# Kernel optimization log

Measured on AMD Instinct MI355X. Metric: run time of the kernel, lower is better.

## Reference

```python
import jax, jax.numpy as jnp
import numpy as np

N_SRC = 100000
N_DST = 100000
N_EDGES = 640000
D = 128
D_OUT = 128


def setup_inputs() -> dict:
    key = jax.random.key(0)
    k1, k2, k3, k4, k5, k6 = jax.random.split(key, 6)
    h_src = jax.random.normal(k1, (N_SRC, D), dtype=jnp.float32)
    h_dst = jax.random.normal(k2, (N_DST, D), dtype=jnp.float32)
    src_idx = jax.random.randint(k3, (N_EDGES,), 0, N_SRC, dtype=jnp.int32)
    dst_idx = jax.random.randint(k4, (N_EDGES,), 0, N_DST, dtype=jnp.int32)
    W = jax.random.normal(k5, (2 * D, D_OUT), dtype=jnp.float32) * 0.05
    b = jax.random.normal(k6, (D_OUT,), dtype=jnp.float32) * 0.05
    return {"h_src": h_src, "h_dst": h_dst, "src_idx": src_idx,
            "dst_idx": dst_idx, "W": W, "b": b}


def reference(h_src, h_dst, src_idx, dst_idx, W, b):
    # copy_u: gather source features along edges -> [E, D]
    msgs = h_src[src_idx]
    # mean aggregation per destination node (segment mean)
    summed = jax.ops.segment_sum(msgs, dst_idx, num_segments=N_DST)  # [N_dst, D]
    deg = jax.ops.segment_sum(jnp.ones((N_EDGES,), dtype=h_src.dtype),
                              dst_idx, num_segments=N_DST)  # [N_dst]
    h_N = summed / jnp.maximum(deg, 1.0)[:, None]
    # concat self + neighbor mean, then linear projection
    h_total = jnp.concatenate([h_dst, h_N], axis=1)  # [N_dst, 2D]
    return h_total @ W + b
```

## Files before the change

### kernel.cpp

```cpp
#include <hip/hip_runtime.h>

#define D 128
#define N_SRC 100000
#define N_DST 100000
#define N_EDGES 640000

#define SCAN_BLK 1024
#define N_SCAN_BLOCKS ((N_DST + SCAN_BLK - 1) / SCAN_BLK)

typedef __attribute__((ext_vector_type(8))) short s8v;
typedef __attribute__((ext_vector_type(4))) float f32x4;

__device__ __forceinline__ unsigned short f2bf(float f) {
    unsigned int u = __float_as_uint(f);
    u += 0x7fffu + ((u >> 16) & 1u);
    return (unsigned short)(u >> 16);
}


__global__ __launch_bounds__(256) void hist_kernel(
    const int* __restrict__ dst_idx, int* __restrict__ counts)
{
    int e = blockIdx.x * 256 + threadIdx.x;
    if (e < N_EDGES) atomicAdd(&counts[dst_idx[e]], 1);
}

__global__ __launch_bounds__(256) void scan_blocks(
    const int* __restrict__ counts, int* __restrict__ row_start,
    int* __restrict__ block_sums)
{
    __shared__ int sh[256];
    const int tid = threadIdx.x;
    const int base = blockIdx.x * SCAN_BLK + tid * 4;
    int v[4];
    int local = 0;
#pragma unroll
    for (int k = 0; k < 4; k++) {
        int idx = base + k;
        v[k] = (idx < N_DST) ? counts[idx] : 0;
        local += v[k];
    }
    sh[tid] = local;
    __syncthreads();
    for (int off = 1; off < 256; off <<= 1) {
        int t = (tid >= off) ? sh[tid - off] : 0;
        __syncthreads();
        sh[tid] += t;
        __syncthreads();
    }
    int run = (tid == 0) ? 0 : sh[tid - 1];
    if (tid == 255) block_sums[blockIdx.x] = sh[255];
#pragma unroll
    for (int k = 0; k < 4; k++) {
        int idx = base + k;
        if (idx < N_DST) row_start[idx] = run;
        run += v[k];
    }
}

__global__ __launch_bounds__(128) void scan_top(
    const int* __restrict__ block_sums, int* __restrict__ block_offsets)
{
    __shared__ int sh[128];
    const int tid = threadIdx.x;
    sh[tid] = (tid < N_SCAN_BLOCKS) ? block_sums[tid] : 0;
    __syncthreads();
    for (int off = 1; off < 128; off <<= 1) {
        int t = (tid >= off) ? sh[tid - off] : 0;
        __syncthreads();
        sh[tid] += t;
        __syncthreads();
    }
    if (tid < N_SCAN_BLOCKS) block_offsets[tid] = (tid == 0) ? 0 : sh[tid - 1];
}

__global__ __launch_bounds__(256) void add_offsets(
    int* __restrict__ row_start, const int* __restrict__ block_offsets,
    int* __restrict__ cursor)
{
    int i = blockIdx.x * 256 + threadIdx.x;
    if (i < N_DST) {
        int v = row_start[i] + block_offsets[i / SCAN_BLK];
        row_start[i] = v;
        cursor[i] = v;
    }
    if (i == 0) row_start[N_DST] = N_EDGES;
}

__global__ __launch_bounds__(256) void scatter_perm(
    const int* __restrict__ src_idx, const int* __restrict__ dst_idx,
    int* __restrict__ cursor, int* __restrict__ edge_src)
{
    int e = blockIdx.x * 256 + threadIdx.x;
    if (e < N_EDGES) {
        int d = dst_idx[e];
        int pos = atomicAdd(&cursor[d], 1);
        edge_src[pos] = src_idx[e];
    }
}

__global__ __launch_bounds__(256) void convert_hdst(
    const float* __restrict__ h_dst, unsigned short* __restrict__ A)
{
    int t = blockIdx.x * 256 + threadIdx.x;
    if (t >= N_DST * 16) return;
    int row = t >> 4;
    int cq = t & 15;
    const float* src = h_dst + (size_t)row * D + cq * 8;
    float4 v0 = *(const float4*)(src);
    float4 v1 = *(const float4*)(src + 4);
    unsigned short o[8];
    o[0] = f2bf(v0.x); o[1] = f2bf(v0.y); o[2] = f2bf(v0.z); o[3] = f2bf(v0.w);
    o[4] = f2bf(v1.x); o[5] = f2bf(v1.y); o[6] = f2bf(v1.z); o[7] = f2bf(v1.w);
    *(s8v*)(A + (size_t)row * 256 + cq * 8) = *(s8v*)o;
}

__global__ __launch_bounds__(256) void pack_W(
    const float* __restrict__ W, unsigned short* __restrict__ Bp)
{
    int id = blockIdx.x * 256 + threadIdx.x;
    if (id >= 32768) return;
    int j = id & 7;
    int l = (id >> 3) & 63;
    int t = (id >> 9) & 7;
    int s = id >> 12;
    int k = s * 32 + (l >> 4) * 8 + j;
    int n = t * 16 + (l & 15);
    Bp[id] = f2bf(W[k * D + n]);
}

__global__ __launch_bounds__(256) void aggregate(
    const float* __restrict__ h_src, const int* __restrict__ row_start,
    const int* __restrict__ edge_src, unsigned int* __restrict__ A32)
{
    const int wave = threadIdx.x >> 6;
    const int lane = threadIdx.x & 63;
    const int row = blockIdx.x * 4 + wave;
    if (row >= N_DST) return;
    const int start = row_start[row];
    const int deg = row_start[row + 1] - start;
    float2 acc = {0.f, 0.f};
    for (int base = 0; base < deg; base += 16) {
        int n = min(16, deg - base);
        int myid = (lane < n) ? edge_src[start + base + lane] : 0;
        for (int t = 0; t < n; t++) {
            int s = __shfl(myid, t);
            float2 v = ((const float2*)(h_src + (size_t)s * D))[lane];
            acc.x += v.x; acc.y += v.y;
        }
    }
    const float inv = 1.0f / fmaxf((float)deg, 1.0f);
    unsigned int packed = (unsigned int)f2bf(acc.x * inv)
                        | ((unsigned int)f2bf(acc.y * inv) << 16);
    A32[(size_t)row * 128 + 64 + lane] = packed;
}

__global__ __launch_bounds__(256, 4) void mfma_gemm(
    const unsigned short* __restrict__ A,
    const unsigned short* __restrict__ Bp,
    const float* __restrict__ bias,
    float* __restrict__ out)
{
    const int wave = threadIdx.x >> 6;
    const int lane = threadIdx.x & 63;
    const int row0 = (blockIdx.x * 4 + wave) * 16;
    if (row0 >= N_DST) return;
    const int quad = lane >> 4;
    const int lr = lane & 15;

    f32x4 acc[8];
#pragma unroll
    for (int t = 0; t < 8; t++) acc[t] = (f32x4){0.f, 0.f, 0.f, 0.f};

    const unsigned short* arow = A + (size_t)(row0 + lr) * 256 + quad * 8;

#pragma unroll
    for (int s = 0; s < 8; s++) {
        s8v a = *(const s8v*)(arow + s * 32);
#pragma unroll
        for (int t = 0; t < 8; t++) {
            s8v bf = *(const s8v*)(Bp + (((size_t)(s * 8 + t) * 64 + lane) * 8));
            acc[t] = __builtin_amdgcn_mfma_f32_16x16x32_bf16(a, bf, acc[t], 0, 0, 0);
        }
    }

#pragma unroll
    for (int t = 0; t < 8; t++) {
        float bv = bias[t * 16 + lr];
#pragma unroll
        for (int r = 0; r < 4; r++) {
            int row = row0 + quad * 4 + r;
            out[(size_t)row * D + t * 16 + lr] = acc[t][r] + bv;
        }
    }
}

extern "C" void kernel_launch(void* const* d_in, const int* in_sizes, int n_in,
                              void* d_out, int out_size, void* d_ws, size_t ws_size,
                              hipStream_t stream) {
    const float* h_src  = (const float*)d_in[0];
    const float* h_dst  = (const float*)d_in[1];
    const int* src_idx  = (const int*)d_in[2];
    const int* dst_idx  = (const int*)d_in[3];
    const float* W      = (const float*)d_in[4];
    const float* b      = (const float*)d_in[5];
    float* out = (float*)d_out;

    unsigned short* Bp = (unsigned short*)d_ws;
    int* ws_i          = (int*)((char*)d_ws + 65536);
    int* row_start     = ws_i;
    int* cursor        = row_start + (N_DST + 1);
    int* counts        = cursor + N_DST;
    int* block_sums    = counts + N_DST;
    int* block_offsets = block_sums + N_SCAN_BLOCKS;
    int* edge_src      = block_offsets + N_SCAN_BLOCKS;

    hipMemsetAsync(counts, 0, (size_t)N_DST * sizeof(int), stream);

    hist_kernel<<<(N_EDGES + 255) / 256, 256, 0, stream>>>(dst_idx, counts);
    scan_blocks<<<N_SCAN_BLOCKS, 256, 0, stream>>>(counts, row_start, block_sums);
    scan_top<<<1, 128, 0, stream>>>(block_sums, block_offsets);
    add_offsets<<<(N_DST + 255) / 256, 256, 0, stream>>>(row_start, block_offsets, cursor);
    scatter_perm<<<(N_EDGES + 255) / 256, 256, 0, stream>>>(src_idx, dst_idx, cursor, edge_src);

    convert_hdst<<<(N_DST * 16 + 255) / 256, 256, 0, stream>>>(
        h_dst, (unsigned short*)d_out);
    pack_W<<<128, 256, 0, stream>>>(W, Bp);

    aggregate<<<N_DST / 4, 256, 0, stream>>>(h_src, row_start, edge_src,
                                             (unsigned int*)d_out);

    int gemm_blocks = (N_DST / 16 + 3) / 4;
    mfma_gemm<<<gemm_blocks, 256, 0, stream>>>(
        (const unsigned short*)d_out, Bp, b, out);
}
```

Measured before the change: 303.7 us.

## Fuse h_dst bf16 conversion into GEMM, widen GEMM tiles, unroll aggregation gather

Drops the separate h_dst to bf16 conversion kernel. The GEMM now reads fp32 h_dst directly and converts it in registers for the first half of K, which avoids writing and re-reading an intermediate bf16 copy. Each GEMM wave now computes 32 rows instead of 16, so every loaded B fragment feeds two MFMAs, at the cost of more accumulator registers. The aggregation loop is fully unrolled in fixed groups of 8 edges with masking, so more gathers are in flight at once; this issues redundant loads for padded edge slots.

Result: faster. 281.3 us (-7.4%).

```diff
diff --git a/kernel.cpp b/kernel.cpp
--- a/kernel.cpp
+++ b/kernel.cpp
@@ -97,22 +97,6 @@
         int pos = atomicAdd(&cursor[d], 1);
         edge_src[pos] = src_idx[e];
     }
-}
-
-__global__ __launch_bounds__(256) void convert_hdst(
-    const float* __restrict__ h_dst, unsigned short* __restrict__ A)
-{
-    int t = blockIdx.x * 256 + threadIdx.x;
-    if (t >= N_DST * 16) return;
-    int row = t >> 4;
-    int cq = t & 15;
-    const float* src = h_dst + (size_t)row * D + cq * 8;
-    float4 v0 = *(const float4*)(src);
-    float4 v1 = *(const float4*)(src + 4);
-    unsigned short o[8];
-    o[0] = f2bf(v0.x); o[1] = f2bf(v0.y); o[2] = f2bf(v0.z); o[3] = f2bf(v0.w);
-    o[4] = f2bf(v1.x); o[5] = f2bf(v1.y); o[6] = f2bf(v1.z); o[7] = f2bf(v1.w);
-    *(s8v*)(A + (size_t)row * 256 + cq * 8) = *(s8v*)o;
 }
 
 __global__ __launch_bounds__(256) void pack_W(
@@ -140,13 +124,16 @@
     const int start = row_start[row];
     const int deg = row_start[row + 1] - start;
     float2 acc = {0.f, 0.f};
-    for (int base = 0; base < deg; base += 16) {
-        int n = min(16, deg - base);
-        int myid = (lane < n) ? edge_src[start + base + lane] : 0;
-        for (int t = 0; t < n; t++) {
+    for (int base = 0; base < deg; base += 8) {
+        int j = base + (lane & 7);
+        int myid = edge_src[start + min(j, deg - 1)];
+#pragma unroll
+        for (int t = 0; t < 8; t++) {
             int s = __shfl(myid, t);
             float2 v = ((const float2*)(h_src + (size_t)s * D))[lane];
-            acc.x += v.x; acc.y += v.y;
+            bool ok = (base + t) < deg;
+            acc.x += ok ? v.x : 0.f;
+            acc.y += ok ? v.y : 0.f;
         }
     }
     const float inv = 1.0f / fmaxf((float)deg, 1.0f);
@@ -156,6 +143,7 @@
 }
 
 __global__ __launch_bounds__(256, 4) void mfma_gemm(
+    const float* __restrict__ h_dst,
     const unsigned short* __restrict__ A,
     const unsigned short* __restrict__ Bp,
     const float* __restrict__ bias,
@@ -163,24 +151,54 @@
 {
     const int wave = threadIdx.x >> 6;
     const int lane = threadIdx.x & 63;
-    const int row0 = (blockIdx.x * 4 + wave) * 16;
+    const int row0 = (blockIdx.x * 4 + wave) * 32;
     if (row0 >= N_DST) return;
     const int quad = lane >> 4;
     const int lr = lane & 15;
-
-    f32x4 acc[8];
-#pragma unroll
-    for (int t = 0; t < 8; t++) acc[t] = (f32x4){0.f, 0.f, 0.f, 0.f};
-
-    const unsigned short* arow = A + (size_t)(row0 + lr) * 256 + quad * 8;
-
-#pragma unroll
-    for (int s = 0; s < 8; s++) {
-        s8v a = *(const s8v*)(arow + s * 32);
+    const int r0 = row0 + lr;
+    const int r1 = row0 + 16 + lr;
+
+    f32x4 acc0[8], acc1[8];
+#pragma unroll
+    for (int t = 0; t < 8; t++) {
+        acc0[t] = (f32x4){0.f, 0.f, 0.f, 0.f};
+        acc1[t] = (f32x4){0.f, 0.f, 0.f, 0.f};
+    }
+
+    const float* p0 = h_dst + (size_t)r0 * D + quad * 8;
+    const float* p1 = h_dst + (size_t)r1 * D + quad * 8;
+    const unsigned short* q0 = A + (size_t)r0 * 256 + 128 + quad * 8;
+    const unsigned short* q1 = A + (size_t)r1 * 256 + 128 + quad * 8;
+
+#pragma unroll
+    for (int s = 0; s < 4; s++) {
+        float4 x0 = *(const float4*)(p0 + s * 32);
+        float4 y0 = *(const float4*)(p0 + s * 32 + 4);
+        float4 x1 = *(const float4*)(p1 + s * 32);
+        float4 y1 = *(const float4*)(p1 + s * 32 + 4);
+        unsigned short a0u[8], a1u[8];
+        a0u[0]=f2bf(x0.x); a0u[1]=f2bf(x0.y); a0u[2]=f2bf(x0.z); a0u[3]=f2bf(x0.w);
+        a0u[4]=f2bf(y0.x); a0u[5]=f2bf(y0.y); a0u[6]=f2bf(y0.z); a0u[7]=f2bf(y0.w);
+        a1u[0]=f2bf(x1.x); a1u[1]=f2bf(x1.y); a1u[2]=f2bf(x1.z); a1u[3]=f2bf(x1.w);
+        a1u[4]=f2bf(y1.x); a1u[5]=f2bf(y1.y); a1u[6]=f2bf(y1.z); a1u[7]=f2bf(y1.w);
+        s8v a0 = *(s8v*)a0u;
+        s8v a1 = *(s8v*)a1u;
 #pragma unroll
         for (int t = 0; t < 8; t++) {
-            s8v bf = *(const s8v*)(Bp + (((size_t)(s * 8 + t) * 64 + lane) * 8));
-            acc[t] = __builtin_amdgcn_mfma_f32_16x16x32_bf16(a, bf, acc[t], 0, 0, 0);
+            s8v bf = *(const s8v*)(Bp + ((size_t)(s * 8 + t) * 64 + lane) * 8);
+            acc0[t] = __builtin_amdgcn_mfma_f32_16x16x32_bf16(a0, bf, acc0[t], 0, 0, 0);
+            acc1[t] = __builtin_amdgcn_mfma_f32_16x16x32_bf16(a1, bf, acc1[t], 0, 0, 0);
+        }
+    }
+#pragma unroll
+    for (int s = 4; s < 8; s++) {
+        s8v a0 = *(const s8v*)(q0 + (s - 4) * 32);
+        s8v a1 = *(const s8v*)(q1 + (s - 4) * 32);
+#pragma unroll
+        for (int t = 0; t < 8; t++) {
+            s8v bf = *(const s8v*)(Bp + ((size_t)(s * 8 + t) * 64 + lane) * 8);
+            acc0[t] = __builtin_amdgcn_mfma_f32_16x16x32_bf16(a0, bf, acc0[t], 0, 0, 0);
+            acc1[t] = __builtin_amdgcn_mfma_f32_16x16x32_bf16(a1, bf, acc1[t], 0, 0, 0);
         }
     }
 
@@ -189,8 +207,10 @@
         float bv = bias[t * 16 + lr];
 #pragma unroll
         for (int r = 0; r < 4; r++) {
-            int row = row0 + quad * 4 + r;
-            out[(size_t)row * D + t * 16 + lr] = acc[t][r] + bv;
+            int rowa = row0 + quad * 4 + r;
+            int rowb = row0 + 16 + quad * 4 + r;
+            out[(size_t)rowa * D + t * 16 + lr] = acc0[t][r] + bv;
+            out[(size_t)rowb * D + t * 16 + lr] = acc1[t][r] + bv;
         }
     }
 }
@@ -223,14 +243,12 @@
     add_offsets<<<(N_DST + 255) / 256, 256, 0, stream>>>(row_start, block_offsets, cursor);
     scatter_perm<<<(N_EDGES + 255) / 256, 256, 0, stream>>>(src_idx, dst_idx, cursor, edge_src);
 
-    convert_hdst<<<(N_DST * 16 + 255) / 256, 256, 0, stream>>>(
-        h_dst, (unsigned short*)d_out);
     pack_W<<<128, 256, 0, stream>>>(W, Bp);
 
     aggregate<<<N_DST / 4, 256, 0, stream>>>(h_src, row_start, edge_src,
                                              (unsigned int*)d_out);
 
-    int gemm_blocks = (N_DST / 16 + 3) / 4;
+    int gemm_blocks = (N_DST / 32 + 3) / 4;
     mfma_gemm<<<gemm_blocks, 256, 0, stream>>>(
-        (const unsigned short*)d_out, Bp, b, out);
-}
+        h_dst, (const unsigned short*)d_out, Bp, b, out);
+}
```
